# Kernel tuning notes

Measured on AMD Instinct MI355X. Metric: run time of the kernel, lower is better.

Reference implementation:

```python
import jax, jax.numpy as jnp
import numpy as np

N_NODES = 50000
N_EDGES = 200000
D_FEAT = 512
D_HID = 1024


def setup_inputs() -> dict:
    key = jax.random.key(0)
    k_x, k_s, k_d, k_w1, k_w2 = jax.random.split(key, 5)
    x = jax.random.normal(k_x, (N_NODES, D_FEAT), dtype=jnp.float32)
    src = jax.random.randint(k_s, (N_EDGES,), 0, N_NODES, dtype=jnp.int64)
    dst = jax.random.randint(k_d, (N_EDGES,), 0, N_NODES, dtype=jnp.int64)
    # MLP params: Linear(2d -> hidden), ReLU, Linear(hidden -> 1)
    W1 = jax.random.normal(k_w1, (2 * D_FEAT, D_HID), dtype=jnp.float32) * (1.0 / np.sqrt(2 * D_FEAT))
    b1 = jnp.zeros((D_HID,), dtype=jnp.float32)
    W2 = jax.random.normal(k_w2, (D_HID, 1), dtype=jnp.float32) * (1.0 / np.sqrt(D_HID))
    b2 = jnp.zeros((1,), dtype=jnp.float32)
    return {"x": x, "src": src, "dst": dst, "W1": W1, "b1": b1, "W2": W2, "b2": b2}


def reference(x, src, dst, W1, b1, W2, b2):
    # Per-edge gather of src/dst node embeddings, concat along feature dim
    h = jnp.concatenate([x[src], x[dst]], axis=1)          # [E, 2d]
    h = jax.nn.relu(h @ W1 + b1)                            # [E, hidden]
    score = h @ W2 + b2                                     # [E, 1]
    return score
```

## Files before the change

kernel.cpp:

```cpp
#include <hip/hip_runtime.h>
#include <cstdint>
#include <cstddef>

typedef __attribute__((ext_vector_type(8))) short short8;
typedef __attribute__((ext_vector_type(4))) float f32x4;

#define D_FEAT 512
#define D_HID  1024
#define NCOL   2048

__device__ __forceinline__ unsigned short f2bf(float f) {
    unsigned u = __builtin_bit_cast(unsigned, f);
    u += 0x7FFFu + ((u >> 16) & 1u);
    return (unsigned short)(u >> 16);
}
__device__ __forceinline__ float bf2f(unsigned short h) {
    unsigned u = ((unsigned)h) << 16;
    return __builtin_bit_cast(float, u);
}

__global__ __launch_bounds__(256) void cast_x_kernel(const float* __restrict__ x,
                                                     unsigned short* __restrict__ xb,
                                                     int n) {
    int i = (blockIdx.x * 256 + threadIdx.x) * 8;
    if (i >= n) return;
    const float4* xp = (const float4*)(x + i);
    float4 a = xp[0], b = xp[1];
    short8 o;
    o[0] = (short)f2bf(a.x); o[1] = (short)f2bf(a.y);
    o[2] = (short)f2bf(a.z); o[3] = (short)f2bf(a.w);
    o[4] = (short)f2bf(b.x); o[5] = (short)f2bf(b.y);
    o[6] = (short)f2bf(b.z); o[7] = (short)f2bf(b.w);
    *(short8*)(xb + i) = o;
}

__global__ __launch_bounds__(256) void transpose_w1_kernel(const float* __restrict__ W1,
                                                           unsigned short* __restrict__ w1t) {
    __shared__ float tile[32][33];
    const int half = blockIdx.z;
    const int kb = blockIdx.y * 32;
    const int nb = blockIdx.x * 32;
    const int tx = threadIdx.x, ty = threadIdx.y;
    #pragma unroll
    for (int i = 0; i < 32; i += 8)
        tile[ty + i][tx] = W1[(size_t)(half * 512 + kb + ty + i) * 1024 + nb + tx];
    __syncthreads();
    #pragma unroll
    for (int i = 0; i < 32; i += 8)
        w1t[(size_t)(half * 1024 + nb + ty + i) * 512 + kb + tx] = f2bf(tile[tx][ty + i]);
}

#define BM 128
#define BN 128
#define BK 64
#define GM 32

__global__ __launch_bounds__(256, 2) void gemm_uv_kernel(
    const unsigned short* __restrict__ xb,
    const unsigned short* __restrict__ w1t,
    const float* __restrict__ b1,
    unsigned short* __restrict__ UV,
    int M, int MB)
{
    __shared__ __align__(16) unsigned short smem[16384];
    unsigned short* sA = smem;
    unsigned short* sB = smem + 8192;

    const int NB = NCOL / BN;
    int bid = blockIdx.x;
    int g    = bid / (GM * NB);
    int rem  = bid - g * (GM * NB);
    int base = g * GM;
    int gm   = MB - base; if (gm > GM) gm = GM;
    int mb   = base + rem % gm;
    int nb   = rem / gm;
    const int m0 = mb * BM;
    const int n0 = nb * BN;

    const int tid  = threadIdx.x;
    const int wave = tid >> 6;
    const int lane = tid & 63;
    const int q    = lane >> 4;
    const int l15  = lane & 15;
    const int wm   = (wave >> 1) * 64;
    const int wn   = (wave & 1) * 64;

    const int ar = lane >> 3;
    const int ac = ((lane & 7) ^ ar) * 8;

    const int swz = l15 & 7;
    const int c0 = (q ^ swz) * 8;
    const int c1 = ((q ^ swz) ^ 4) * 8;

    f32x4 zero = {0.f, 0.f, 0.f, 0.f};
    f32x4 acc[4][4];
    #pragma unroll
    for (int i = 0; i < 4; ++i)
        #pragma unroll
        for (int j = 0; j < 4; ++j)
            acc[i][j] = zero;

    #pragma unroll 1
    for (int kt = 0; kt < 8; ++kt) {
        const int k0 = kt * BK;
        __syncthreads();
        #pragma unroll
        for (int i = 0; i < 4; ++i) {
            int slot = wave * 4 + i;
            int row  = slot * 8 + ar;
            int m    = m0 + row; if (m >= M) m = M - 1;
            __builtin_amdgcn_global_load_lds(
                (const __attribute__((address_space(1))) void*)(xb + (size_t)m * D_FEAT + k0 + ac),
                (__attribute__((address_space(3))) void*)(sA + slot * 512),
                16, 0, 0);
        }
        #pragma unroll
        for (int i = 0; i < 4; ++i) {
            int slot = wave * 4 + i;
            int row  = slot * 8 + ar;
            __builtin_amdgcn_global_load_lds(
                (const __attribute__((address_space(1))) void*)(w1t + (size_t)(n0 + row) * D_FEAT + k0 + ac),
                (__attribute__((address_space(3))) void*)(sB + slot * 512),
                16, 0, 0);
        }
        __syncthreads();
        {
            short8 a[4], b[4];
            #pragma unroll
            for (int mt = 0; mt < 4; ++mt)
                a[mt] = *(const short8*)(sA + (wm + mt * 16 + l15) * 64 + c0);
            #pragma unroll
            for (int nt = 0; nt < 4; ++nt)
                b[nt] = *(const short8*)(sB + (wn + nt * 16 + l15) * 64 + c0);
            #pragma unroll
            for (int mt = 0; mt < 4; ++mt)
                #pragma unroll
                for (int nt = 0; nt < 4; ++nt)
                    acc[mt][nt] = __builtin_amdgcn_mfma_f32_16x16x32_bf16(a[mt], b[nt], acc[mt][nt], 0, 0, 0);
            #pragma unroll
            for (int mt = 0; mt < 4; ++mt)
                a[mt] = *(const short8*)(sA + (wm + mt * 16 + l15) * 64 + c1);
            #pragma unroll
            for (int nt = 0; nt < 4; ++nt)
                b[nt] = *(const short8*)(sB + (wn + nt * 16 + l15) * 64 + c1);
            #pragma unroll
            for (int mt = 0; mt < 4; ++mt)
                #pragma unroll
                for (int nt = 0; nt < 4; ++nt)
                    acc[mt][nt] = __builtin_amdgcn_mfma_f32_16x16x32_bf16(a[mt], b[nt], acc[mt][nt], 0, 0, 0);
        }
    }

    float b1v[4];
    #pragma unroll
    for (int nt = 0; nt < 4; ++nt) {
        int n = n0 + wn + nt * 16 + l15;
        b1v[nt] = (n < D_HID) ? b1[n] : 0.f;
    }
    __syncthreads();
    unsigned short* ep = smem + wave * 4096;
    #pragma unroll
    for (int mt = 0; mt < 4; ++mt)
        #pragma unroll
        for (int nt = 0; nt < 4; ++nt)
            #pragma unroll
            for (int r = 0; r < 4; ++r) {
                float v = acc[mt][nt][r] + b1v[nt];
                ep[(mt * 16 + q * 4 + r) * 64 + nt * 16 + l15] = f2bf(v);
            }
    __syncthreads();
    #pragma unroll
    for (int i = 0; i < 8; ++i) {
        int flat = i * 64 + lane;
        int r  = flat >> 3;
        int c8 = (flat & 7) * 8;
        int m  = m0 + wm + r;
        if (m < M) {
            short8 v = *(const short8*)(ep + r * 64 + c8);
            *(short8*)(UV + (size_t)m * NCOL + n0 + wn + c8) = v;
        }
    }
}

__global__ __launch_bounds__(256) void edge_score_kernel(
    const unsigned short* __restrict__ UV,
    const int* __restrict__ src, const int* __restrict__ dst,
    const float* __restrict__ W2, const float* __restrict__ b2,
    float* __restrict__ out, int E)
{
    const int wave = threadIdx.x >> 6;
    const int lane = threadIdx.x & 63;
    const int gw = blockIdx.x * 4 + wave;
    const int e0 = gw * 2;
    const int e1 = e0 + 1;
    if (e0 >= E) return;
    const bool has1 = (e1 < E);

    const int s0 = src[e0];
    const int d0 = dst[e0];
    const int s1 = has1 ? src[e1] : s0;
    const int d1 = has1 ? dst[e1] : d0;

    const unsigned short* up0 = UV + (size_t)s0 * NCOL + lane * 16;
    const unsigned short* vp0 = UV + (size_t)d0 * NCOL + D_HID + lane * 16;
    const unsigned short* up1 = UV + (size_t)s1 * NCOL + lane * 16;
    const unsigned short* vp1 = UV + (size_t)d1 * NCOL + D_HID + lane * 16;

    short8 a0 = *(const short8*)up0;
    short8 a1 = *(const short8*)(up0 + 8);
    short8 b0 = *(const short8*)vp0;
    short8 b1 = *(const short8*)(vp0 + 8);
    short8 c0 = *(const short8*)up1;
    short8 c1 = *(const short8*)(up1 + 8);
    short8 d0v = *(const short8*)vp1;
    short8 d1v = *(const short8*)(vp1 + 8);

    const float4* wp = (const float4*)(W2 + lane * 16);
    float4 wa = wp[0], wb = wp[1], wc = wp[2], wd = wp[3];
    float w[16] = {wa.x, wa.y, wa.z, wa.w, wb.x, wb.y, wb.z, wb.w,
                   wc.x, wc.y, wc.z, wc.w, wd.x, wd.y, wd.z, wd.w};
    const float bias = b2[0];

    float acc0 = 0.f, acc1 = 0.f;
    #pragma unroll
    for (int k = 0; k < 8; ++k) {
        float h0 = bf2f((unsigned short)a0[k]) + bf2f((unsigned short)b0[k]);
        acc0 = fmaf(fmaxf(h0, 0.f), w[k], acc0);
        float h1 = bf2f((unsigned short)c0[k]) + bf2f((unsigned short)d0v[k]);
        acc1 = fmaf(fmaxf(h1, 0.f), w[k], acc1);
    }
    #pragma unroll
    for (int k = 0; k < 8; ++k) {
        float h0 = bf2f((unsigned short)a1[k]) + bf2f((unsigned short)b1[k]);
        acc0 = fmaf(fmaxf(h0, 0.f), w[8 + k], acc0);
        float h1 = bf2f((unsigned short)c1[k]) + bf2f((unsigned short)d1v[k]);
        acc1 = fmaf(fmaxf(h1, 0.f), w[8 + k], acc1);
    }
    #pragma unroll
    for (int off = 1; off < 64; off <<= 1) {
        acc0 += __shfl_xor(acc0, off);
        acc1 += __shfl_xor(acc1, off);
    }
    if (lane == 0) out[e0] = acc0 + bias;
    if (lane == 1 && has1) out[e1] = acc1 + bias;
}

extern "C" void kernel_launch(void* const* d_in, const int* in_sizes, int n_in,
                              void* d_out, int out_size, void* d_ws, size_t ws_size,
                              hipStream_t stream) {
    const float* x   = (const float*)d_in[0];
    const int*   src = (const int*)d_in[1];
    const int*   dst = (const int*)d_in[2];
    const float* W1  = (const float*)d_in[3];
    const float* b1  = (const float*)d_in[4];
    const float* W2  = (const float*)d_in[5];
    const float* b2  = (const float*)d_in[6];
    float* out = (float*)d_out;

    const int M = in_sizes[0] / D_FEAT;
    const int E = in_sizes[1];

    char* ws = (char*)d_ws;
    unsigned short* UV  = (unsigned short*)ws;
    unsigned short* xb  = (unsigned short*)(ws + (size_t)M * NCOL * 2);
    unsigned short* w1t = (unsigned short*)(ws + (size_t)M * NCOL * 2 + (size_t)M * D_FEAT * 2);

    const int nx = M * D_FEAT;
    cast_x_kernel<<<(nx / 8 + 255) / 256, 256, 0, stream>>>(x, xb, nx);
    transpose_w1_kernel<<<dim3(32, 16, 2), dim3(32, 8), 0, stream>>>(W1, w1t);
    const int MB = (M + BM - 1) / BM;
    gemm_uv_kernel<<<MB * (NCOL / BN), 256, 0, stream>>>(xb, w1t, b1, UV, M, MB);
    edge_score_kernel<<<(E + 7) / 8, 256, 0, stream>>>(UV, src, dst, W2, b2, out, E);
}
```

Measured before the change: 375.2 us.

## Quantize intermediate UV projections to int8 with per-chunk row scales

The GEMM epilogue now quantizes each row's 64-column chunk of the node projections to int8 with an fp32 absmax scale, in place of storing bf16. The edge kernel gathers int8 data plus scales and dequantizes before the ReLU and the dot with W2. This halves the bytes written by the GEMM and the bytes gathered per edge, cutting memory traffic in both stages. In exchange it adds quantization error beyond bf16, plus extra shuffles and scale loads.

```diff
diff --git a/kernel.cpp b/kernel.cpp
--- a/kernel.cpp
+++ b/kernel.cpp
@@ -8,15 +8,15 @@
 #define D_FEAT 512
 #define D_HID  1024
 #define NCOL   2048
+#define NCHUNK 32
 
 __device__ __forceinline__ unsigned short f2bf(float f) {
     unsigned u = __builtin_bit_cast(unsigned, f);
     u += 0x7FFFu + ((u >> 16) & 1u);
     return (unsigned short)(u >> 16);
 }
-__device__ __forceinline__ float bf2f(unsigned short h) {
-    unsigned u = ((unsigned)h) << 16;
-    return __builtin_bit_cast(float, u);
+__device__ __forceinline__ float i8f(int w, int b) {
+    return (float)((int)(w << (24 - 8 * b)) >> 24);
 }
 
 __global__ __launch_bounds__(256) void cast_x_kernel(const float* __restrict__ x,
@@ -59,7 +59,8 @@
     const unsigned short* __restrict__ xb,
     const unsigned short* __restrict__ w1t,
     const float* __restrict__ b1,
-    unsigned short* __restrict__ UV,
+    signed char* __restrict__ qUV,
+    float* __restrict__ scales,
     int M, int MB)
 {
     __shared__ __align__(16) unsigned short smem[16384];
@@ -157,33 +158,66 @@
         int n = n0 + wn + nt * 16 + l15;
         b1v[nt] = (n < D_HID) ? b1[n] : 0.f;
     }
+    #pragma unroll
+    for (int mt = 0; mt < 4; ++mt)
+        #pragma unroll
+        for (int nt = 0; nt < 4; ++nt)
+            #pragma unroll
+            for (int r = 0; r < 4; ++r)
+                acc[mt][nt][r] += b1v[nt];
+
+    float sc[4][4], inv[4][4];
+    #pragma unroll
+    for (int mt = 0; mt < 4; ++mt)
+        #pragma unroll
+        for (int r = 0; r < 4; ++r) {
+            float m_ = fmaxf(fmaxf(fabsf(acc[mt][0][r]), fabsf(acc[mt][1][r])),
+                             fmaxf(fabsf(acc[mt][2][r]), fabsf(acc[mt][3][r])));
+            #pragma unroll
+            for (int off = 1; off < 16; off <<= 1)
+                m_ = fmaxf(m_, __shfl_xor(m_, off));
+            sc[mt][r]  = m_ * (1.0f / 127.0f);
+            inv[mt][r] = (m_ > 0.f) ? (127.0f / m_) : 0.f;
+        }
+
     __syncthreads();
-    unsigned short* ep = smem + wave * 4096;
+    char* ep8 = (char*)smem + wave * 4096;
     #pragma unroll
     for (int mt = 0; mt < 4; ++mt)
         #pragma unroll
         for (int nt = 0; nt < 4; ++nt)
             #pragma unroll
             for (int r = 0; r < 4; ++r) {
-                float v = acc[mt][nt][r] + b1v[nt];
-                ep[(mt * 16 + q * 4 + r) * 64 + nt * 16 + l15] = f2bf(v);
+                float qv = rintf(acc[mt][nt][r] * inv[mt][r]);
+                qv = fminf(fmaxf(qv, -127.f), 127.f);
+                ep8[(mt * 16 + q * 4 + r) * 64 + nt * 16 + l15] = (signed char)(int)qv;
             }
-    __syncthreads();
-    #pragma unroll
-    for (int i = 0; i < 8; ++i) {
+    const int chunk = (n0 + wn) >> 6;
+    if (l15 == 0) {
+        #pragma unroll
+        for (int mt = 0; mt < 4; ++mt)
+            #pragma unroll
+            for (int r = 0; r < 4; ++r) {
+                int m = m0 + wm + mt * 16 + q * 4 + r;
+                if (m < M) scales[(size_t)m * NCHUNK + chunk] = sc[mt][r];
+            }
+    }
+    #pragma unroll
+    for (int i = 0; i < 4; ++i) {
         int flat = i * 64 + lane;
-        int r  = flat >> 3;
-        int c8 = (flat & 7) * 8;
-        int m  = m0 + wm + r;
+        int r   = flat >> 2;
+        int c16 = (flat & 3) * 16;
+        int m   = m0 + wm + r;
         if (m < M) {
-            short8 v = *(const short8*)(ep + r * 64 + c8);
-            *(short8*)(UV + (size_t)m * NCOL + n0 + wn + c8) = v;
+            int4 v = *(const int4*)(ep8 + r * 64 + c16);
+            *(int4*)(qUV + (size_t)m * NCOL + n0 + wn + c16) = v;
         }
     }
 }
 
 __global__ __launch_bounds__(256) void edge_score_kernel(
-    const unsigned short* __restrict__ UV,
+    const signed char* __restrict__ qUV,
+    const float* __restrict__ scales,
     const int* __restrict__ src, const int* __restrict__ dst,
     const float* __restrict__ W2, const float* __restrict__ b2,
     float* __restrict__ out, int E)
@@ -201,19 +235,15 @@
     const int s1 = has1 ? src[e1] : s0;
     const int d1 = has1 ? dst[e1] : d0;
 
-    const unsigned short* up0 = UV + (size_t)s0 * NCOL + lane * 16;
-    const unsigned short* vp0 = UV + (size_t)d0 * NCOL + D_HID + lane * 16;
-    const unsigned short* up1 = UV + (size_t)s1 * NCOL + lane * 16;
-    const unsigned short* vp1 = UV + (size_t)d1 * NCOL + D_HID + lane * 16;
-
-    short8 a0 = *(const short8*)up0;
-    short8 a1 = *(const short8*)(up0 + 8);
-    short8 b0 = *(const short8*)vp0;
-    short8 b1 = *(const short8*)(vp0 + 8);
-    short8 c0 = *(const short8*)up1;
-    short8 c1 = *(const short8*)(up1 + 8);
-    short8 d0v = *(const short8*)vp1;
-    short8 d1v = *(const short8*)(vp1 + 8);
+    int4 qu0 = *(const int4*)(qUV + (size_t)s0 * NCOL + lane * 16);
+    int4 qv0 = *(const int4*)(qUV + (size_t)d0 * NCOL + D_HID + lane * 16);
+    int4 qu1 = *(const int4*)(qUV + (size_t)s1 * NCOL + lane * 16);
+    int4 qv1 = *(const int4*)(qUV + (size_t)d1 * NCOL + D_HID + lane * 16);
+    const int ch = lane >> 2;
+    float su0 = scales[(size_t)s0 * NCHUNK + ch];
+    float sv0 = scales[(size_t)d0 * NCHUNK + 16 + ch];
+    float su1 = scales[(size_t)s1 * NCHUNK + ch];
+    float sv1 = scales[(size_t)d1 * NCHUNK + 16 + ch];
 
     const float4* wp = (const float4*)(W2 + lane * 16);
     float4 wa = wp[0], wb = wp[1], wc = wp[2], wd = wp[3];
@@ -221,20 +251,20 @@
                    wc.x, wc.y, wc.z, wc.w, wd.x, wd.y, wd.z, wd.w};
     const float bias = b2[0];
 
+    const int* u0w = (const int*)&qu0; const int* v0w = (const int*)&qv0;
+    const int* u1w = (const int*)&qu1; const int* v1w = (const int*)&qv1;
+
     float acc0 = 0.f, acc1 = 0.f;
     #pragma unroll
-    for (int k = 0; k < 8; ++k) {
-        float h0 = bf2f((unsigned short)a0[k]) + bf2f((unsigned short)b0[k]);
-        acc0 = fmaf(fmaxf(h0, 0.f), w[k], acc0);
-        float h1 = bf2f((unsigned short)c0[k]) + bf2f((unsigned short)d0v[k]);
-        acc1 = fmaf(fmaxf(h1, 0.f), w[k], acc1);
-    }
-    #pragma unroll
-    for (int k = 0; k < 8; ++k) {
-        float h0 = bf2f((unsigned short)a1[k]) + bf2f((unsigned short)b1[k]);
-        acc0 = fmaf(fmaxf(h0, 0.f), w[8 + k], acc0);
-        float h1 = bf2f((unsigned short)c1[k]) + bf2f((unsigned short)d1v[k]);
-        acc1 = fmaf(fmaxf(h1, 0.f), w[8 + k], acc1);
+    for (int dw = 0; dw < 4; ++dw) {
+        #pragma unroll
+        for (int b = 0; b < 4; ++b) {
+            int k = dw * 4 + b;
+            float h0 = fmaf(i8f(u0w[dw], b), su0, i8f(v0w[dw], b) * sv0);
+            acc0 = fmaf(fmaxf(h0, 0.f), w[k], acc0);
+            float h1 = fmaf(i8f(u1w[dw], b), su1, i8f(v1w[dw], b) * sv1);
+            acc1 = fmaf(fmaxf(h1, 0.f), w[k], acc1);
+        }
     }
     #pragma unroll
     for (int off = 1; off < 64; off <<= 1) {
@@ -261,14 +291,16 @@
     const int E = in_sizes[1];
 
     char* ws = (char*)d_ws;
-    unsigned short* UV  = (unsigned short*)ws;
-    unsigned short* xb  = (unsigned short*)(ws + (size_t)M * NCOL * 2);
-    unsigned short* w1t = (unsigned short*)(ws + (size_t)M * NCOL * 2 + (size_t)M * D_FEAT * 2);
+    signed char*   qUV    = (signed char*)ws;
+    float*         scales = (float*)(ws + (size_t)M * NCOL);
+    unsigned short* xb    = (unsigned short*)(ws + (size_t)M * NCOL + (size_t)M * NCHUNK * 4);
+    unsigned short* w1t   = (unsigned short*)(ws + (size_t)M * NCOL + (size_t)M * NCHUNK * 4
+                                                 + (size_t)M * D_FEAT * 2);
 
     const int nx = M * D_FEAT;
     cast_x_kernel<<<(nx / 8 + 255) / 256, 256, 0, stream>>>(x, xb, nx);
     transpose_w1_kernel<<<dim3(32, 16, 2), dim3(32, 8), 0, stream>>>(W1, w1t);
     const int MB = (M + BM - 1) / BM;
-    gemm_uv_kernel<<<MB * (NCOL / BN), 256, 0, stream>>>(xb, w1t, b1, UV, M, MB);
-    edge_score_kernel<<<(E + 7) / 8, 256, 0, stream>>>(UV, src, dst, W2, b2, out, E);
-}
+    gemm_uv_kernel<<<MB * (NCOL / BN), 256, 0, stream>>>(xb, w1t, b1, qUV, scales, M, MB);
+    edge_score_kernel<<<(E + 7) / 8, 256, 0, stream>>>(qUV, scales, src, dst, W2, b2, out, E);
+}
```

New measurement: 365.3 us. 1.03x faster.
